# Performance work log

Hardware: AMD Instinct MI355X
Metric: run time of the kernel (lower is better)

The kernel has to match this reference:

```python
import jax, jax.numpy as jnp
import numpy as np

N_NODES = 100000
N_EDGES = 1600000
NUM_GRAPHS = 1000
NODE_IN, EDGE_IN = 32, 16
NODE_EMB, EDGE_EMB, HID, OUT, L = 64, 32, 64, 1, 3
EPS = 1e-5


def _glorot(key, shape):
    fan_in = shape[0]
    return jax.random.normal(key, shape, jnp.float32) / np.sqrt(fan_in)


def setup_inputs() -> dict:
    key = jax.random.key(0)
    ks = jax.random.split(key, 16)
    inp = {
        "x": jax.random.normal(ks[0], (N_NODES, NODE_IN), jnp.float32),
        "edge_attr": jax.random.normal(ks[1], (N_EDGES, EDGE_IN), jnp.float32),
        "edge_index": jax.random.randint(ks[2], (2, N_EDGES), 0, N_NODES, jnp.int64
                                         if jax.config.jax_enable_x64 else jnp.int32),
        "batch": jnp.sort(jax.random.randint(ks[3], (N_NODES,), 0, NUM_GRAPHS)),
        # embeddings
        "node_W": _glorot(ks[4], (NODE_IN, NODE_EMB)),
        "node_b": jnp.zeros((NODE_EMB,), jnp.float32),
        "edge_W": _glorot(ks[5], (EDGE_IN, EDGE_EMB)),
        "edge_b": jnp.zeros((EDGE_EMB,), jnp.float32),
        # per-layer MPNN params (node_dim==64 for every layer since node_emb_dim==hidden_dim)
        "msg_W": _glorot(ks[6], (L, NODE_EMB + EDGE_EMB, HID)),
        "msg_b": jnp.zeros((L, HID), jnp.float32),
        "msg_gamma": jnp.ones((L, HID), jnp.float32),
        "msg_beta": jnp.zeros((L, HID), jnp.float32),
        "upd_W": _glorot(ks[7], (L, NODE_EMB + HID, HID)),
        "upd_b": jnp.zeros((L, HID), jnp.float32),
        "upd_gamma": jnp.ones((L, HID), jnp.float32),
        "upd_beta": jnp.zeros((L, HID), jnp.float32),
        # readout
        "r1_W": _glorot(ks[8], (HID, HID)),
        "r1_b": jnp.zeros((HID,), jnp.float32),
        "r2_W": _glorot(ks[9], (HID, OUT)),
        "r2_b": jnp.zeros((OUT,), jnp.float32),
    }
    return inp


def _bn(h, gamma, beta):
    # BatchNorm1d in training mode: normalize with batch mean / biased variance
    mu = jnp.mean(h, axis=0)
    var = jnp.mean(jnp.square(h - mu), axis=0)
    return gamma * (h - mu) * jax.lax.rsqrt(var + EPS) + beta


def reference(x, edge_attr, edge_index, batch,
              node_W, node_b, edge_W, edge_b,
              msg_W, msg_b, msg_gamma, msg_beta,
              upd_W, upd_b, upd_gamma, upd_beta,
              r1_W, r1_b, r2_W, r2_b):
    h = x @ node_W + node_b                       # [N, 64]
    e = edge_attr @ edge_W + edge_b               # [E, 32]
    src, dst = edge_index[0], edge_index[1]
    for i in range(L):
        # message: gather x_j, concat edge feats, Linear-ReLU-BN (dropout = eval/no-op)
        m = jnp.concatenate([h[src], e], axis=-1) @ msg_W[i] + msg_b[i]   # [E, 64]
        m = _bn(jax.nn.relu(m), msg_gamma[i], msg_beta[i])
        # aggregate: scatter-add to destination nodes
        agg = jax.ops.segment_sum(m, dst, num_segments=N_NODES)          # [N, 64]
        # update: concat self feats, Linear-ReLU-BN
        u = jnp.concatenate([h, agg], axis=-1) @ upd_W[i] + upd_b[i]     # [N, 64]
        h = _bn(jax.nn.relu(u), upd_gamma[i], upd_beta[i])
    # global add pool over graphs
    g = jax.ops.segment_sum(h, batch, num_segments=NUM_GRAPHS)           # [G, 64]
    out = jax.nn.relu(g @ r1_W + r1_b) @ r2_W + r2_b                     # [G, 1]
    return out
```

## Files before the change

kernel.cpp:

```cpp
#include <hip/hip_runtime.h>
#include <hip/hip_bf16.h>

#define N_NODES   100000
#define N_EDGES   1600000
#define NUM_GRAPHS 1000

typedef unsigned int u32;
typedef unsigned short u16;

typedef __bf16 bf16_t;
typedef bf16_t bf16x8 __attribute__((ext_vector_type(8)));
typedef float  f32x4  __attribute__((ext_vector_type(4)));
typedef u32    u32x4  __attribute__((ext_vector_type(4)));

__device__ __forceinline__ float bf2f(u16 u){ return __uint_as_float(((u32)u)<<16); }
__device__ __forceinline__ float BL(u32 u){ return __uint_as_float(u<<16); }
__device__ __forceinline__ float BH(u32 u){ return __uint_as_float(u&0xffff0000u); }
__device__ __forceinline__ u16 f2bf(float f){
  u32 u = __float_as_uint(f);
  return (u16)((u + 0x7fffu + ((u>>16)&1u)) >> 16);
}
__device__ __forceinline__ float ldf(const void* p, size_t i, int isbf){
  return isbf ? bf2f(((const u16*)p)[i]) : ((const float*)p)[i];
}
__device__ __forceinline__ uint4 ntload4(const void* p){
  u32x4 v = __builtin_nontemporal_load((const u32x4*)p);
  return make_uint4(v.x, v.y, v.z, v.w);
}

union U4BF { uint4 u; bf16x8 v; };

__global__ void k_detect(const u32* __restrict__ x, int* __restrict__ flag){
  int t = threadIdx.x; int cnt = 0;
  for (int i = t; i < 256; i += 64){
    u32 w = x[i];
    u32 e = (w >> 7) & 0xffu;
    if (e >= 110u && e <= 137u) cnt++;
  }
  for (int o = 32; o; o >>= 1) cnt += __shfl_xor(cnt, o);
  if (t == 0) *flag = (cnt > 128) ? 1 : 0;
}

__global__ void k_idaff(float* __restrict__ haff){
  int c = threadIdx.x;
  haff[c] = 1.f; haff[64 + c] = 0.f;
}

__global__ void k_prep(const void* __restrict__ eW, const void* __restrict__ eb,
                       const void* __restrict__ mW, const void* __restrict__ mb,
                       u16* __restrict__ Weff, float* __restrict__ biasm,
                       const int* __restrict__ flagp){
  int isbf = *flagp;
  int l = blockIdx.x, c = threadIdx.x;
  u16* W = Weff + ((size_t)l*64 + c)*96;
  for (int k = 0; k < 64; k++)
    W[k] = f2bf(ldf(mW, (size_t)(l*96 + k)*64 + c, isbf));
  for (int j = 0; j < 16; j++){
    float acc = 0.f;
    for (int k = 0; k < 32; k++)
      acc += ldf(eW, (size_t)j*32 + k, isbf) * ldf(mW, (size_t)(l*96 + 64 + k)*64 + c, isbf);
    W[64 + j] = f2bf(acc);
  }
  float fbv = ldf(mb, (size_t)l*64 + c, isbf);
  for (int k = 0; k < 32; k++)
    fbv += ldf(eb, k, isbf) * ldf(mW, (size_t)(l*96 + 64 + k)*64 + c, isbf);
  W[80] = f2bf(fbv);
  biasm[(size_t)l*64 + c] = fbv;
  for (int k = 81; k < 96; k++) W[k] = 0;
}

__global__ void k_fold(const void* __restrict__ mW, const u16* __restrict__ Wbase,
                       const float* __restrict__ biasm, const float* __restrict__ haff,
                       u16* __restrict__ Wf, const int* __restrict__ flagp, int l){
  int isbf = *flagp; int c = threadIdx.x;
  const u16* Wb = Wbase + ((size_t)l*64 + c)*96;
  u16* W = Wf + (size_t)c*96;
  float bb = biasm[(size_t)l*64 + c];
  for (int k = 0; k < 64; k++){
    float w = ldf(mW, (size_t)(l*96 + k)*64 + c, isbf);
    W[k] = f2bf(haff[k] * w);
    bb = fmaf(haff[64 + k], w, bb);
  }
  for (int k = 64; k < 80; k++) W[k] = Wb[k];
  W[80] = f2bf(bb);
  for (int k = 81; k < 96; k++) W[k] = 0;
}

__global__ void k_updprep(const void* __restrict__ uW, const void* __restrict__ ub,
                          const float* __restrict__ maff, const float* __restrict__ haff,
                          u16* __restrict__ Wupd, float* __restrict__ biasv,
                          float* __restrict__ tvv, const int* __restrict__ flagp, int l){
  int isbf = *flagp; int c = threadIdx.x;
  u16* W = Wupd + (size_t)c*192;
  float tv = 0.f, bb = 0.f;
  for (int k = 0; k < 64; k++){
    float wka = ldf(uW, (size_t)(l*128 + k)*64 + c, isbf);
    W[k] = f2bf(haff[k] * wka);
    bb = fmaf(haff[64 + k], wka, bb);
    float wkb = ldf(uW, (size_t)(l*128 + 64 + k)*64 + c, isbf);
    float prod = wkb * maff[k];
    u16 hi = f2bf(prod);
    W[64 + k]  = hi;
    W[128 + k] = f2bf(prod - bf2f(hi));
    tv = fmaf(maff[64 + k], wkb, tv);
  }
  biasv[c] = ldf(ub, (size_t)l*64 + c, isbf) + bb;
  tvv[c] = tv;
}

__global__ void k_node_emb(const void* __restrict__ x, const void* __restrict__ nW,
                           const void* __restrict__ nb, u16* __restrict__ hsp,
                           const int* __restrict__ flagp){
  int isbf = *flagp;
  int lane = threadIdx.x & 63;
  int gw = (blockIdx.x*blockDim.x + threadIdx.x) >> 6;
  int nw = (gridDim.x*blockDim.x) >> 6;
  float w[32];
#pragma unroll
  for (int k = 0; k < 32; k++) w[k] = ldf(nW, (size_t)k*64 + lane, isbf);
  float bias = ldf(nb, lane, isbf);
  for (int n = gw; n < N_NODES; n += nw){
    float acc = bias;
    if (isbf){
      const uint4* xr = (const uint4*)((const u16*)x + (size_t)n*32);
#pragma unroll
      for (int q = 0; q < 4; q++){
        uint4 a = xr[q];
        u32 uu[4] = {a.x, a.y, a.z, a.w};
#pragma unroll
        for (int j = 0; j < 4; j++){
          acc = fmaf(BL(uu[j]), w[q*8 + 2*j + 0], acc);
          acc = fmaf(BH(uu[j]), w[q*8 + 2*j + 1], acc);
        }
      }
    } else {
      const float4* xr = (const float4*)((const float*)x + (size_t)n*32);
#pragma unroll
      for (int q = 0; q < 8; q++){
        float4 a = xr[q];
        acc = fmaf(a.x, w[q*4+0], acc); acc = fmaf(a.y, w[q*4+1], acc);
        acc = fmaf(a.z, w[q*4+2], acc); acc = fmaf(a.w, w[q*4+3], acc);
      }
    }
    u16 hi = f2bf(acc);
    hsp[(size_t)n*128 + lane]      = hi;
    hsp[(size_t)n*128 + 64 + lane] = f2bf(acc - bf2f(hi));
  }
}

__global__ void k_deg(const int* __restrict__ ei, int* __restrict__ deg){
  int i = blockIdx.x*blockDim.x + threadIdx.x;
  int stride = gridDim.x*blockDim.x;
  for (int e = i; e < N_EDGES; e += stride)
    atomicAdd(&deg[ei[N_EDGES + e]], 1);
}

__global__ void __launch_bounds__(256) k_scan1(const int* __restrict__ deg,
                                               int* __restrict__ bsum){
  __shared__ int wsum[4];
  int b = blockIdx.x, t = threadIdx.x;
  int i0 = b*512 + t;
  int s = 0;
  if (i0 < N_NODES) s += deg[i0];
  if (i0 + 256 < N_NODES) s += deg[i0 + 256];
  for (int o = 32; o; o >>= 1) s += __shfl_xor(s, o);
  if ((t & 63) == 0) wsum[t >> 6] = s;
  __syncthreads();
  if (t == 0) bsum[b] = wsum[0] + wsum[1] + wsum[2] + wsum[3];
}

__global__ void k_scan2(const int* __restrict__ bsum, int* __restrict__ boff,
                        int* __restrict__ rp){
  __shared__ int l[200];
  int t = threadIdx.x;
  if (t < 196) l[t] = bsum[t];
  __syncthreads();
  if (t == 0){
    int r = 0;
    for (int k = 0; k < 196; k++){ int x = l[k]; l[k] = r; r += x; }
    rp[N_NODES] = r;
  }
  __syncthreads();
  if (t < 196) boff[t] = l[t];
}

__global__ void __launch_bounds__(256) k_scan3(const int* __restrict__ deg,
                        const int* __restrict__ boff, int* __restrict__ rp,
                        int* __restrict__ cursor, float* __restrict__ degf){
  __shared__ int wpre[4];
  int b = blockIdx.x, t = threadIdx.x;
  int i0 = b*512 + 2*t;
  int d0 = (i0     < N_NODES) ? deg[i0]     : 0;
  int d1 = (i0 + 1 < N_NODES) ? deg[i0 + 1] : 0;
  int s = d0 + d1;
  int incl = s;
  for (int o = 1; o < 64; o <<= 1){ int u = __shfl_up(incl, o); if ((t & 63) >= o) incl += u; }
  if ((t & 63) == 63) wpre[t >> 6] = incl;
  __syncthreads();
  if (t == 0){ int r = 0; for (int k = 0; k < 4; k++){ int x = wpre[k]; wpre[k] = r; r += x; } }
  __syncthreads();
  int excl = boff[b] + wpre[t >> 6] + incl - s;
  if (i0 < N_NODES){
    rp[i0] = excl; cursor[i0] = excl; degf[i0] = (float)d0;
  }
  if (i0 + 1 < N_NODES){
    rp[i0+1] = excl + d0; cursor[i0+1] = excl + d0; degf[i0+1] = (float)d1;
  }
}

__global__ void k_ranges(const int* __restrict__ rp, int* __restrict__ wr,
                         int nwaves){
  int w = blockIdx.x*blockDim.x + threadIdx.x;
  if (w > nwaves) return;
  if (w == nwaves){ wr[w] = N_NODES; return; }
  long long t0 = (long long)w * N_EDGES / nwaves;
  int lo = 0, hi = N_NODES;
  while (lo < hi){ int mid = (lo+hi)>>1; if ((long long)rp[mid] < t0) lo = mid+1; else hi = mid; }
  wr[w] = lo;
}

__global__ void k_scatter(const int* __restrict__ ei, int* __restrict__ cursor,
                          int* __restrict__ perm2){
  int i = blockIdx.x*blockDim.x + threadIdx.x;
  int stride = gridDim.x*blockDim.x;
  for (int e = i; e < N_EDGES; e += stride){
    int d = ei[N_EDGES + e];
    int p = atomicAdd(&cursor[d], 1);
    ((int2*)perm2)[p] = make_int2(ei[e], e);
  }
}

__global__ void k_scatter2(const int* __restrict__ ei, int* __restrict__ cursor,
                           int* __restrict__ perm, u16* __restrict__ eacsr,
                           const void* __restrict__ ea, const int* __restrict__ flagp){
  int isbf = *flagp;
  int i = blockIdx.x*blockDim.x + threadIdx.x;
  int stride = gridDim.x*blockDim.x;
  if (i < 16){
    perm[N_EDGES + i] = 0;
    uint4 z = make_uint4(0,0,0,0);
    uint4* out = (uint4*)(eacsr + (size_t)(N_EDGES + i)*16);
    out[0] = z; out[1] = z;
  }
  for (int e = i; e < N_EDGES; e += stride){
    int d = ei[N_EDGES + e];
    int p = atomicAdd(&cursor[d], 1);
    perm[p] = ei[e];
    uint4 r0, r1;
    if (isbf){
      const uint4* er = (const uint4*)((const u16*)ea + (size_t)e*16);
      r0 = er[0]; r1 = er[1];
    } else {
      const float4* ef = (const float4*)((const float*)ea + (size_t)e*16);
      float4 f0 = ef[0], f1 = ef[1], f2 = ef[2], f3 = ef[3];
      r0.x = (u32)f2bf(f0.x) | ((u32)f2bf(f0.y)<<16);
      r0.y = (u32)f2bf(f0.z) | ((u32)f2bf(f0.w)<<16);
      r0.z = (u32)f2bf(f1.x) | ((u32)f2bf(f1.y)<<16);
      r0.w = (u32)f2bf(f1.z) | ((u32)f2bf(f1.w)<<16);
      r1.x = (u32)f2bf(f2.x) | ((u32)f2bf(f2.y)<<16);
      r1.y = (u32)f2bf(f2.z) | ((u32)f2bf(f2.w)<<16);
      r1.z = (u32)f2bf(f3.x) | ((u32)f2bf(f3.y)<<16);
      r1.w = (u32)f2bf(f3.z) | ((u32)f2bf(f3.w)<<16);
    }
    uint4* out = (uint4*)(eacsr + (size_t)p*16);
    out[0] = r0; out[1] = r1;
  }
}

__device__ __forceinline__ void adv_tile(const int* __restrict__ rp,
                                         int ni, int bi, int ei,
                                         int& no, int& bo, int& eo){
  if (bi + 16 < ei){ no = ni; bo = bi + 16; eo = ei; return; }
  int t = ni + 1;
  int nb = ei;
  int ne = rp[(t < N_NODES) ? t + 1 : N_NODES];
  while (nb == ne && t + 1 < N_NODES){
    t++; nb = ne; ne = rp[t + 1];
  }
  no = t; bo = nb; eo = ne;
}

__global__ void __launch_bounds__(256) k_msgmm(
    const u16* __restrict__ hsp, const void* __restrict__ ea,
    const int* __restrict__ rp, const int* __restrict__ perm2,
    const u16* __restrict__ Wl, u16* __restrict__ aggs,
    float* __restrict__ stats, const int* __restrict__ flagp,
    int nwaves){
  __shared__ float bs[128];
  int tid = threadIdx.x;
  if (tid < 128) bs[tid] = 0.f;
  __syncthreads();
  int isbf = *flagp;
  int lane = tid & 63, wv = tid >> 6;
  int w = blockIdx.x*4 + wv;
  long long t0 = (long long)w     * N_EDGES / nwaves;
  long long t1 = (long long)(w+1) * N_EDGES / nwaves;
  int lo = 0, hi = N_NODES;
  while (lo < hi){ int mid = (lo+hi)>>1; if ((long long)rp[mid] < t0) lo = mid+1; else hi = mid; }
  int n0 = lo, n1;
  if (w == nwaves-1) n1 = N_NODES;
  else {
    lo = 0; hi = N_NODES;
    while (lo < hi){ int mid = (lo+hi)>>1; if ((long long)rp[mid] < t1) lo = mid+1; else hi = mid; }
    n1 = lo;
  }
  int nn = lane & 15, kg = lane >> 4;
  bf16x8 B[3][4];
#pragma unroll
  for (int t = 0; t < 4; t++)
#pragma unroll
    for (int kb = 0; kb < 3; kb++)
      B[kb][t] = *(const bf16x8*)(Wl + (size_t)(t*16+nn)*96 + kb*32 + kg*8);
  U4BF ac; ac.u = make_uint4((kg==2)? 0x3f80u : 0u, 0u, 0u, 0u);
  float s1[4] = {0,0,0,0}, s2[4] = {0,0,0,0};
  for (int n = n0; n < n1; n++){
    int b0 = rp[n], b1 = rp[n+1];
    float r0 = 0.f, r1 = 0.f, r2 = 0.f, r3 = 0.f;
    for (int base = b0; base < b1; base += 16){
      int rem = b1 - base; if (rem > 16) rem = 16;
      int row = (nn < rem) ? nn : rem-1;
      int2 p = ((const int2*)perm2)[base + row];
      const uint4* hp = (const uint4*)(hsp + (size_t)p.x*128);
      U4BF fA, fB, fC;
      fA.u = hp[kg];
      fB.u = hp[4 + kg];
      if (kg < 2){
        if (isbf){
          fC.u = ((const uint4*)ea)[(size_t)p.y*2 + kg];
        } else {
          const float4* ef = (const float4*)ea;
          float4 f0 = ef[(size_t)p.y*4 + kg*2];
          float4 f1 = ef[(size_t)p.y*4 + kg*2 + 1];
          fC.u.x = (u32)f2bf(f0.x) | ((u32)f2bf(f0.y)<<16);
          fC.u.y = (u32)f2bf(f0.z) | ((u32)f2bf(f0.w)<<16);
          fC.u.z = (u32)f2bf(f1.x) | ((u32)f2bf(f1.y)<<16);
          fC.u.w = (u32)f2bf(f1.z) | ((u32)f2bf(f1.w)<<16);
        }
      } else fC = ac;
      f32x4 a0 = {0,0,0,0}, a1 = {0,0,0,0}, a2 = {0,0,0,0}, a3 = {0,0,0,0};
      a0 = __builtin_amdgcn_mfma_f32_16x16x32_bf16(fA.v, B[0][0], a0, 0,0,0);
      a1 = __builtin_amdgcn_mfma_f32_16x16x32_bf16(fA.v, B[0][1], a1, 0,0,0);
      a2 = __builtin_amdgcn_mfma_f32_16x16x32_bf16(fA.v, B[0][2], a2, 0,0,0);
      a3 = __builtin_amdgcn_mfma_f32_16x16x32_bf16(fA.v, B[0][3], a3, 0,0,0);
      a0 = __builtin_amdgcn_mfma_f32_16x16x32_bf16(fB.v, B[1][0], a0, 0,0,0);
      a1 = __builtin_amdgcn_mfma_f32_16x16x32_bf16(fB.v, B[1][1], a1, 0,0,0);
      a2 = __builtin_amdgcn_mfma_f32_16x16x32_bf16(fB.v, B[1][2], a2, 0,0,0);
      a3 = __builtin_amdgcn_mfma_f32_16x16x32_bf16(fB.v, B[1][3], a3, 0,0,0);
      a0 = __builtin_amdgcn_mfma_f32_16x16x32_bf16(fC.v, B[2][0], a0, 0,0,0);
      a1 = __builtin_amdgcn_mfma_f32_16x16x32_bf16(fC.v, B[2][1], a1, 0,0,0);
      a2 = __builtin_amdgcn_mfma_f32_16x16x32_bf16(fC.v, B[2][2], a2, 0,0,0);
      a3 = __builtin_amdgcn_mfma_f32_16x16x32_bf16(fC.v, B[2][3], a3, 0,0,0);
      int rowbase = kg*4;
      float ts0 = 0.f, ts1 = 0.f, ts2 = 0.f, ts3 = 0.f;
#pragma unroll
      for (int j = 0; j < 4; j++){
        bool valid = (rowbase + j) < rem;
        float m0 = fmaxf(a0[j], 0.f); m0 = valid ? m0 : 0.f;
        float m1 = fmaxf(a1[j], 0.f); m1 = valid ? m1 : 0.f;
        float m2 = fmaxf(a2[j], 0.f); m2 = valid ? m2 : 0.f;
        float m3 = fmaxf(a3[j], 0.f); m3 = valid ? m3 : 0.f;
        ts0 += m0; ts1 += m1; ts2 += m2; ts3 += m3;
        s2[0] = fmaf(m0,m0,s2[0]); s2[1] = fmaf(m1,m1,s2[1]);
        s2[2] = fmaf(m2,m2,s2[2]); s2[3] = fmaf(m3,m3,s2[3]);
      }
      s1[0] += ts0; s1[1] += ts1; s1[2] += ts2; s1[3] += ts3;
      ts0 += __shfl_xor(ts0,16); ts0 += __shfl_xor(ts0,32);
      ts1 += __shfl_xor(ts1,16); ts1 += __shfl_xor(ts1,32);
      ts2 += __shfl_xor(ts2,16); ts2 += __shfl_xor(ts2,32);
      ts3 += __shfl_xor(ts3,16); ts3 += __shfl_xor(ts3,32);
      r0 += ts0; r1 += ts1; r2 += ts2; r3 += ts3;
    }
    float v = (kg==0) ? r0 : (kg==1) ? r1 : (kg==2) ? r2 : r3;
    u16 hiv = f2bf(v);
    aggs[(size_t)n*128 + lane]      = hiv;
    aggs[(size_t)n*128 + 64 + lane] = f2bf(v - bf2f(hiv));
  }
#pragma unroll
  for (int t = 0; t < 4; t++){
    atomicAdd(&bs[t*16+nn], s1[t]);
    atomicAdd(&bs[64+t*16+nn], s2[t]);
  }
  __syncthreads();
  if (tid < 128) atomicAdd(&stats[tid], bs[tid]);
}

__global__ void __launch_bounds__(256) k_msgmm2(
    const u16* __restrict__ hsp, const u16* __restrict__ eacsr,
    const int* __restrict__ rp, const int* __restrict__ perm,
    const u16* __restrict__ Wl, u16* __restrict__ aggs,
    float* __restrict__ stats, const int* __restrict__ wranges){
  __shared__ float bs[128];
  int tid = threadIdx.x;
  if (tid < 128) bs[tid] = 0.f;
  __syncthreads();
  int lane = tid & 63;
  int w = blockIdx.x*4 + (tid >> 6);
  int nBeg = wranges[w], nEnd = wranges[w+1];
  int nn = lane & 15, kg = lane >> 4;
  bf16x8 B[3][4];
#pragma unroll
  for (int t = 0; t < 4; t++)
#pragma unroll
    for (int kb = 0; kb < 3; kb++)
      B[kb][t] = *(const bf16x8*)(Wl + (size_t)(t*16+nn)*96 + kb*32 + kg*8);
  U4BF ac; ac.u = make_uint4((kg==2)? 0x3f80u : 0u, 0u, 0u, 0u);
  float s1[4] = {0,0,0,0}, s2[4] = {0,0,0,0};

  if (nBeg < nEnd){
    {
      int pv = rp[nBeg];
      for (int m = nBeg; m < nEnd; m++){
        int nx = rp[m+1];
        if (nx == pv){
          aggs[(size_t)m*128 + lane] = 0;
          aggs[(size_t)m*128 + 64 + lane] = 0;
        }
        pv = nx;
      }
    }
    int nA = nBeg;
    int baseA = rp[nA], b1A = rp[nA+1];
    while (baseA == b1A && nA + 1 < nEnd){ nA++; baseA = b1A; b1A = rp[nA+1]; }
    if (baseA < b1A){
      int nB, baseB, b1B;
      adv_tile(rp, nA, baseA, b1A, nB, baseB, b1B);
      int pB = __builtin_nontemporal_load(&perm[baseB + nn]);
      U4BF fAA, fAB, fAC;
      {
        int pA = __builtin_nontemporal_load(&perm[baseA + nn]);
        const uint4* hpA = (const uint4*)(hsp + (size_t)pA*128);
        fAA.u = hpA[kg]; fAB.u = hpA[4 + kg];
        if (kg < 2) fAC.u = ntload4(eacsr + ((size_t)baseA + nn)*16 + (size_t)kg*8);
        else fAC = ac;
      }
      float r0 = 0.f, r1 = 0.f, r2 = 0.f, r3 = 0.f;
      while (true){
        int nC, baseC, b1C;
        adv_tile(rp, nB, baseB, b1B, nC, baseC, b1C);
        int pC = __builtin_nontemporal_load(&perm[baseC + nn]);
        const uint4* hpB = (const uint4*)(hsp + (size_t)pB*128);
        U4BF fBA, fBB, fBC;
        fBA.u = hpB[kg]; fBB.u = hpB[4 + kg];
        if (kg < 2) fBC.u = ntload4(eacsr + ((size_t)baseB + nn)*16 + (size_t)kg*8);
        else fBC = ac;
        f32x4 a0 = {0,0,0,0}, a1 = {0,0,0,0}, a2 = {0,0,0,0}, a3 = {0,0,0,0};
        a0 = __builtin_amdgcn_mfma_f32_16x16x32_bf16(fAA.v, B[0][0], a0, 0,0,0);
        a1 = __builtin_amdgcn_mfma_f32_16x16x32_bf16(fAA.v, B[0][1], a1, 0,0,0);
        a2 = __builtin_amdgcn_mfma_f32_16x16x32_bf16(fAA.v, B[0][2], a2, 0,0,0);
        a3 = __builtin_amdgcn_mfma_f32_16x16x32_bf16(fAA.v, B[0][3], a3, 0,0,0);
        a0 = __builtin_amdgcn_mfma_f32_16x16x32_bf16(fAB.v, B[1][0], a0, 0,0,0);
        a1 = __builtin_amdgcn_mfma_f32_16x16x32_bf16(fAB.v, B[1][1], a1, 0,0,0);
        a2 = __builtin_amdgcn_mfma_f32_16x16x32_bf16(fAB.v, B[1][2], a2, 0,0,0);
        a3 = __builtin_amdgcn_mfma_f32_16x16x32_bf16(fAB.v, B[1][3], a3, 0,0,0);
        a0 = __builtin_amdgcn_mfma_f32_16x16x32_bf16(fAC.v, B[2][0], a0, 0,0,0);
        a1 = __builtin_amdgcn_mfma_f32_16x16x32_bf16(fAC.v, B[2][1], a1, 0,0,0);
        a2 = __builtin_amdgcn_mfma_f32_16x16x32_bf16(fAC.v, B[2][2], a2, 0,0,0);
        a3 = __builtin_amdgcn_mfma_f32_16x16x32_bf16(fAC.v, B[2][3], a3, 0,0,0);
        int rem = b1A - baseA; if (rem > 16) rem = 16;
        int rowbase = kg*4;
        float ts0 = 0.f, ts1 = 0.f, ts2 = 0.f, ts3 = 0.f;
#pragma unroll
        for (int j = 0; j < 4; j++){
          bool valid = (rowbase + j) < rem;
          float m0 = fmaxf(a0[j], 0.f); m0 = valid ? m0 : 0.f;
          float m1 = fmaxf(a1[j], 0.f); m1 = valid ? m1 : 0.f;
          float m2 = fmaxf(a2[j], 0.f); m2 = valid ? m2 : 0.f;
          float m3 = fmaxf(a3[j], 0.f); m3 = valid ? m3 : 0.f;
          ts0 += m0; ts1 += m1; ts2 += m2; ts3 += m3;
          s2[0] = fmaf(m0,m0,s2[0]); s2[1] = fmaf(m1,m1,s2[1]);
          s2[2] = fmaf(m2,m2,s2[2]); s2[3] = fmaf(m3,m3,s2[3]);
        }
        s1[0] += ts0; s1[1] += ts1; s1[2] += ts2; s1[3] += ts3;
        r0 += ts0; r1 += ts1; r2 += ts2; r3 += ts3;
        if (baseA + 16 >= b1A){
          r0 += __shfl_xor(r0,16); r0 += __shfl_xor(r0,32);
          r1 += __shfl_xor(r1,16); r1 += __shfl_xor(r1,32);
          r2 += __shfl_xor(r2,16); r2 += __shfl_xor(r2,32);
          r3 += __shfl_xor(r3,16); r3 += __shfl_xor(r3,32);
          float v = (kg==0) ? r0 : (kg==1) ? r1 : (kg==2) ? r2 : r3;
          u16 hiv = f2bf(v);
          aggs[(size_t)nA*128 + lane]      = hiv;
          aggs[(size_t)nA*128 + 64 + lane] = f2bf(v - bf2f(hiv));
          r0 = r1 = r2 = r3 = 0.f;
        }
        nA = nB; baseA = baseB; b1A = b1B;
        fAA = fBA; fAB = fBB; fAC = fBC;
        nB = nC; baseB = baseC; b1B = b1C; pB = pC;
        if (nA >= nEnd) break;
      }
    }
  }
#pragma unroll
  for (int t = 0; t < 4; t++){
    atomicAdd(&bs[t*16+nn], s1[t]);
    atomicAdd(&bs[64+t*16+nn], s2[t]);
  }
  __syncthreads();
  if (tid < 128) atomicAdd(&stats[tid], bs[tid]);
}

__global__ void k_fin(float* __restrict__ stats, const void* __restrict__ gamma,
                      const void* __restrict__ beta, float* __restrict__ aff,
                      float cnt_inv, int goff, const int* __restrict__ flagp){
  int isbf = *flagp; int c = threadIdx.x;
  float mu  = stats[c]      * cnt_inv;
  float var = stats[64 + c] * cnt_inv - mu*mu;
  float rs  = rsqrtf(var + 1e-5f);
  float g = ldf(gamma, (size_t)goff + c, isbf);
  float b = ldf(beta,  (size_t)goff + c, isbf);
  aff[c]      = g*rs;
  aff[64 + c] = b - g*mu*rs;
  stats[c] = 0.f; stats[64 + c] = 0.f;
}

#define UPD_TILES (N_NODES/16)
__global__ void __launch_bounds__(256) k_updmm(
    const u16* __restrict__ hsp, u16* __restrict__ aggs,
    const float* __restrict__ degf, const u16* __restrict__ Wupd,
    const float* __restrict__ biasv, const float* __restrict__ tvv,
    float* __restrict__ stats){
  __shared__ float bs[128];
  int tid = threadIdx.x;
  if (tid < 128) bs[tid] = 0.f;
  __syncthreads();
  int lane = tid & 63;
  int nn = lane & 15, kg = lane >> 4;
  int w = blockIdx.x*4 + (tid >> 6);
  int nwv = gridDim.x*4;
  bf16x8 B[6][4];
#pragma unroll
  for (int t = 0; t < 4; t++)
#pragma unroll
    for (int kb = 0; kb < 6; kb++)
      B[kb][t] = *(const bf16x8*)(Wupd + (size_t)(t*16+nn)*192 + kb*32 + kg*8);
  float bc[4], tc[4];
#pragma unroll
  for (int t = 0; t < 4; t++){ bc[t] = biasv[t*16+nn]; tc[t] = tvv[t*16+nn]; }
  float s1[4] = {0,0,0,0}, s2[4] = {0,0,0,0};
  for (int tile = w; tile < UPD_TILES; tile += nwv){
    int n0 = tile*16;
    int r = n0 + nn;
    const uint4* hp = (const uint4*)hsp;
    const uint4* ap = (const uint4*)aggs;
    U4BF hh0, hh1, hl0, hl1, ah0, ah1, al0, al1;
    hh0.u = ntload4(&hp[(size_t)r*16 + kg]);       hh1.u = ntload4(&hp[(size_t)r*16 + 4 + kg]);
    hl0.u = ntload4(&hp[(size_t)r*16 + 8 + kg]);   hl1.u = ntload4(&hp[(size_t)r*16 + 12 + kg]);
    ah0.u = ntload4(&ap[(size_t)r*16 + kg]);       ah1.u = ntload4(&ap[(size_t)r*16 + 4 + kg]);
    al0.u = ntload4(&ap[(size_t)r*16 + 8 + kg]);   al1.u = ntload4(&ap[(size_t)r*16 + 12 + kg]);
    float dg[4];
#pragma unroll
    for (int j = 0; j < 4; j++) dg[j] = degf[n0 + kg*4 + j];
    f32x4 a0 = {0,0,0,0}, a1 = {0,0,0,0}, a2 = {0,0,0,0}, a3 = {0,0,0,0};
#define MF(F,KB) \
    a0 = __builtin_amdgcn_mfma_f32_16x16x32_bf16(F.v, B[KB][0], a0, 0,0,0); \
    a1 = __builtin_amdgcn_mfma_f32_16x16x32_bf16(F.v, B[KB][1], a1, 0,0,0); \
    a2 = __builtin_amdgcn_mfma_f32_16x16x32_bf16(F.v, B[KB][2], a2, 0,0,0); \
    a3 = __builtin_amdgcn_mfma_f32_16x16x32_bf16(F.v, B[KB][3], a3, 0,0,0);
    MF(hh0,0) MF(hh1,1) MF(hl0,0) MF(hl1,1)
    MF(ah0,2) MF(ah1,3) MF(ah0,4) MF(ah1,5)
    MF(al0,2) MF(al1,3)
#undef MF
#pragma unroll
    for (int j = 0; j < 4; j++){
      int n = n0 + kg*4 + j;
      float m0 = fmaxf(fmaf(tc[0], dg[j], a0[j] + bc[0]), 0.f);
      float m1 = fmaxf(fmaf(tc[1], dg[j], a1[j] + bc[1]), 0.f);
      float m2 = fmaxf(fmaf(tc[2], dg[j], a2[j] + bc[2]), 0.f);
      float m3 = fmaxf(fmaf(tc[3], dg[j], a3[j] + bc[3]), 0.f);
      s1[0] += m0; s1[1] += m1; s1[2] += m2; s1[3] += m3;
      s2[0] = fmaf(m0,m0,s2[0]); s2[1] = fmaf(m1,m1,s2[1]);
      s2[2] = fmaf(m2,m2,s2[2]); s2[3] = fmaf(m3,m3,s2[3]);
      u16* hw = aggs + (size_t)n*128;
      u16 q0 = f2bf(m0), q1 = f2bf(m1), q2 = f2bf(m2), q3 = f2bf(m3);
      hw[     nn] = q0;  hw[64 +      nn] = f2bf(m0 - bf2f(q0));
      hw[16 + nn] = q1;  hw[64 + 16 + nn] = f2bf(m1 - bf2f(q1));
      hw[32 + nn] = q2;  hw[64 + 32 + nn] = f2bf(m2 - bf2f(q2));
      hw[48 + nn] = q3;  hw[64 + 48 + nn] = f2bf(m3 - bf2f(q3));
    }
  }
#pragma unroll
  for (int t = 0; t < 4; t++){
    atomicAdd(&bs[t*16+nn], s1[t]);
    atomicAdd(&bs[64+t*16+nn], s2[t]);
  }
  __syncthreads();
  if (tid < 128) atomicAdd(&stats[tid], bs[tid]);
}

__global__ void k_pool(const u16* __restrict__ hsp, const int* __restrict__ batch,
                       const float* __restrict__ aff, float* __restrict__ g){
  int lane = threadIdx.x & 63;
  int gw = (blockIdx.x*blockDim.x + threadIdx.x) >> 6;
  int nw = (gridDim.x*blockDim.x) >> 6;
  float s = aff[lane], t = aff[64 + lane];
  int chunk = (N_NODES + nw - 1) / nw;
  int n0 = gw*chunk;
  int n1 = n0 + chunk; if (n1 > N_NODES) n1 = N_NODES;
  int cur = -1; float acc = 0.f, cnt = 0.f;
  for (int n = n0; n < n1; n++){
    int b = batch[n];
    float v = bf2f(hsp[(size_t)n*128 + lane]) + bf2f(hsp[(size_t)n*128 + 64 + lane]);
    if (b != cur){
      if (cur >= 0) atomicAdd(&g[(size_t)cur*64 + lane], fmaf(s, acc, t*cnt));
      cur = b; acc = v; cnt = 1.f;
    } else { acc += v; cnt += 1.f; }
  }
  if (cur >= 0) atomicAdd(&g[(size_t)cur*64 + lane], fmaf(s, acc, t*cnt));
}

__global__ void k_read(const float* __restrict__ g, const void* __restrict__ r1W,
                       const void* __restrict__ r1b, const void* __restrict__ r2W,
                       const void* __restrict__ r2b, void* __restrict__ out,
                       const int* __restrict__ flagp){
  int isbf = *flagp;
  int lane = threadIdx.x;
  int gr = blockIdx.x;
  float w[64];
#pragma unroll
  for (int k = 0; k < 64; k++) w[k] = ldf(r1W, (size_t)k*64 + lane, isbf);
  float acc = ldf(r1b, lane, isbf);
  const float4* grow = (const float4*)(g + (size_t)gr*64);
#pragma unroll
  for (int q = 0; q < 16; q++){
    float4 a = grow[q];
    acc = fmaf(a.x, w[4*q+0], acc); acc = fmaf(a.y, w[4*q+1], acc);
    acc = fmaf(a.z, w[4*q+2], acc); acc = fmaf(a.w, w[4*q+3], acc);
  }
  float hid = fmaxf(acc, 0.f);
  float p = hid * ldf(r2W, lane, isbf);
  for (int o = 32; o; o >>= 1) p += __shfl_xor(p, o);
  if (lane == 0){
    float v = p + ldf(r2b, 0, isbf);
    if (isbf) ((__hip_bfloat16*)out)[gr] = __float2bfloat16(v);
    else      ((float*)out)[gr] = v;
  }
}

extern "C" void kernel_launch(void* const* d_in, const int* in_sizes, int n_in,
                              void* d_out, int out_size, void* d_ws, size_t ws_size,
                              hipStream_t stream){
  const void* x    = d_in[0];
  const void* ea   = d_in[1];
  const int*  ei   = (const int*)d_in[2];
  const int*  bt   = (const int*)d_in[3];
  const void* nW   = d_in[4];  const void* nb  = d_in[5];
  const void* eW   = d_in[6];  const void* eb  = d_in[7];
  const void* mW   = d_in[8];  const void* mb  = d_in[9];
  const void* mg   = d_in[10]; const void* mbe = d_in[11];
  const void* uW   = d_in[12]; const void* ub  = d_in[13];
  const void* ug   = d_in[14]; const void* ube = d_in[15];
  const void* r1W  = d_in[16]; const void* r1b = d_in[17];
  const void* r2W  = d_in[18]; const void* r2b = d_in[19];

  const size_t NEED_BIG = 110768044ull;
  const bool big = (ws_size >= NEED_BIG);

  float* ws = (float*)d_ws;
  size_t off = 0;
  auto alloc = [&](size_t n){ float* p = ws + off; off += n; return p; };

  u16*   hsp   = (u16*)alloc(6400000);
  u16*   aggs  = (u16*)alloc(6400000);
  u16*   eacsr = nullptr; int* perm = nullptr; int* perm2 = nullptr;
  if (big){
    eacsr = (u16*)alloc(12800128);
    perm  = (int*)alloc(1600016);
  } else {
    perm2 = (int*)alloc(3200000);
  }
  float* degf   = alloc(100000);
  float* zero0  = ws + off;
  int*   deg_i  = (int*)alloc(100000);
  float* g      = alloc(64000);
  float* mstats = alloc(128);
  float* ustats = alloc(128);
  size_t zeroN  = (size_t)((ws + off) - zero0);
  float* maff   = alloc(128);
  float* haff   = alloc(128);
  int*   flag   = (int*)alloc(16);
  u16*   Weff   = (u16*)alloc(9216);
  u16*   Wfold  = (u16*)alloc(3072);
  u16*   Wupd   = (u16*)alloc(6144);
  float* biasm  = alloc(192);
  float* biasv  = alloc(64);
  float* tvv    = alloc(64);
  int*   row_ptr= (int*)alloc(100001);
  int*   cursor = (int*)alloc(100000);
  int*   bsum   = (int*)alloc(196);
  int*   boff   = (int*)alloc(196);
  int*   wrng   = (int*)alloc(8194);

  const int MM_BLOCKS = 2048;
  const int MM_WAVES  = MM_BLOCKS * 4;
  const int UPD_BLOCKS = 782;

  k_detect<<<1, 64, 0, stream>>>((const u32*)x, flag);
  hipMemsetAsync(zero0, 0, zeroN*sizeof(float), stream);
  k_idaff<<<1, 64, 0, stream>>>(haff);
  k_prep<<<3, 64, 0, stream>>>(eW, eb, mW, mb, Weff, biasm, flag);
  k_node_emb<<<256, 256, 0, stream>>>(x, nW, nb, hsp, flag);
  k_deg<<<512, 256, 0, stream>>>(ei, deg_i);
  k_scan1<<<196, 256, 0, stream>>>(deg_i, bsum);
  k_scan2<<<1, 256, 0, stream>>>(bsum, boff, row_ptr);
  k_scan3<<<196, 256, 0, stream>>>(deg_i, boff, row_ptr, cursor, degf);
  if (big){
    k_ranges<<<33, 256, 0, stream>>>(row_ptr, wrng, MM_WAVES);
    k_scatter2<<<512, 256, 0, stream>>>(ei, cursor, perm, eacsr, ea, flag);
  } else {
    k_scatter<<<512, 256, 0, stream>>>(ei, cursor, perm2);
  }

  u16* H = hsp;
  u16* G = aggs;
  for (int l = 0; l < 3; l++){
    k_fold<<<1, 64, 0, stream>>>(mW, Weff, biasm, haff, Wfold, flag, l);
    if (big)
      k_msgmm2<<<MM_BLOCKS, 256, 0, stream>>>(H, eacsr, row_ptr, perm, Wfold,
                                              G, mstats, wrng);
    else
      k_msgmm<<<MM_BLOCKS, 256, 0, stream>>>(H, ea, row_ptr, perm2, Wfold,
                                             G, mstats, flag, MM_WAVES);
    k_fin<<<1, 64, 0, stream>>>(mstats, mg, mbe, maff, 1.0f/(float)N_EDGES, l*64, flag);
    k_updprep<<<1, 64, 0, stream>>>(uW, ub, maff, haff, Wupd, biasv, tvv, flag, l);
    k_updmm<<<UPD_BLOCKS, 256, 0, stream>>>(H, G, degf, Wupd, biasv, tvv, ustats);
    k_fin<<<1, 64, 0, stream>>>(ustats, ug, ube, haff, 1.0f/(float)N_NODES, l*64, flag);
    u16* tmp = H; H = G; G = tmp;
  }

  k_pool<<<128, 256, 0, stream>>>(H, bt, haff, g);
  k_read<<<NUM_GRAPHS, 64, 0, stream>>>(g, r1W, r1b, r2W, r2b, d_out, flag);
}
```

Baseline: 1.368 ms.

## Precompute per-wave 16-edge tile lists for the message GEMM loop

Adds three setup kernels that count, prefix-scan and fill a packed list of 16-edge tiles per wave, each entry holding node id, row count and a last-tile flag. The message kernel then walks this flat list instead of advancing through row_ptr with the adv_tile logic, which removes dependent row_ptr loads and branching from the inner pipelined loop. It also swaps the nontemporal loads for plain loads and pads the perm and edge-attribute buffers further so prefetches two tiles ahead stay in bounds. The cost is three extra small launches, a larger workspace requirement and a serial scan in one block.

```diff
diff --git a/kernel.cpp b/kernel.cpp
--- a/kernel.cpp
+++ b/kernel.cpp
@@ -219,6 +219,59 @@
   wr[w] = lo;
 }
 
+
+__global__ void k_tcnt(const int* __restrict__ rp, const int* __restrict__ wr,
+                       int* __restrict__ tcnt, int nwaves){
+  int w = blockIdx.x*blockDim.x + threadIdx.x;
+  if (w >= nwaves) return;
+  int n0 = wr[w], n1 = wr[w+1];
+  int c = 0;
+  for (int n = n0; n < n1; n++){
+    int d = rp[n+1] - rp[n];
+    c += (d + 15) >> 4;
+  }
+  tcnt[w] = c;
+}
+
+__global__ void k_tscan(const int* __restrict__ tcnt, int* __restrict__ twoff,
+                        int nwaves){
+  __shared__ int ps[256];
+  int t = threadIdx.x;
+  int s = 0;
+  for (int i = 0; i < 32; i++) s += tcnt[t*32 + i];
+  ps[t] = s;
+  __syncthreads();
+  if (t == 0){
+    int r = 0;
+    for (int k = 0; k < 256; k++){ int x = ps[k]; ps[k] = r; r += x; }
+    twoff[nwaves] = r;
+  }
+  __syncthreads();
+  int off = ps[t];
+  for (int i = 0; i < 32; i++){
+    twoff[t*32 + i] = off;
+    off += tcnt[t*32 + i];
+  }
+}
+
+__global__ void k_tfill(const int* __restrict__ rp, const int* __restrict__ wr,
+                        const int* __restrict__ twoff, int* __restrict__ tlist,
+                        int nwaves){
+  int w = blockIdx.x*blockDim.x + threadIdx.x;
+  if (w >= nwaves) return;
+  int n0 = wr[w], n1 = wr[w+1];
+  int o = twoff[w];
+  for (int n = n0; n < n1; n++){
+    int b = rp[n], e = rp[n+1];
+    while (b < e){
+      int rem = e - b; if (rem > 16) rem = 16;
+      int last = (b + 16 >= e) ? 1 : 0;
+      tlist[o++] = (n << 5) | ((rem - 1) << 1) | last;
+      b += 16;
+    }
+  }
+}
+
 __global__ void k_scatter(const int* __restrict__ ei, int* __restrict__ cursor,
                           int* __restrict__ perm2){
   int i = blockIdx.x*blockDim.x + threadIdx.x;
@@ -236,7 +289,7 @@
   int isbf = *flagp;
   int i = blockIdx.x*blockDim.x + threadIdx.x;
   int stride = gridDim.x*blockDim.x;
-  if (i < 16){
+  if (i < 48){
     perm[N_EDGES + i] = 0;
     uint4 z = make_uint4(0,0,0,0);
     uint4* out = (uint4*)(eacsr + (size_t)(N_EDGES + i)*16);
@@ -384,18 +437,18 @@
   if (tid < 128) atomicAdd(&stats[tid], bs[tid]);
 }
 
-__global__ void __launch_bounds__(256) k_msgmm2(
+__global__ void __launch_bounds__(256) k_msgmm3(
     const u16* __restrict__ hsp, const u16* __restrict__ eacsr,
     const int* __restrict__ rp, const int* __restrict__ perm,
     const u16* __restrict__ Wl, u16* __restrict__ aggs,
-    float* __restrict__ stats, const int* __restrict__ wranges){
+    float* __restrict__ stats, const int* __restrict__ wranges,
+    const int* __restrict__ twoff, const int* __restrict__ tlist){
   __shared__ float bs[128];
   int tid = threadIdx.x;
   if (tid < 128) bs[tid] = 0.f;
   __syncthreads();
   int lane = tid & 63;
   int w = blockIdx.x*4 + (tid >> 6);
-  int nBeg = wranges[w], nEnd = wranges[w+1];
   int nn = lane & 15, kg = lane >> 4;
   bf16x8 B[3][4];
 #pragma unroll
@@ -406,88 +459,88 @@
   U4BF ac; ac.u = make_uint4((kg==2)? 0x3f80u : 0u, 0u, 0u, 0u);
   float s1[4] = {0,0,0,0}, s2[4] = {0,0,0,0};
 
+  int nBeg = wranges[w], nEnd = wranges[w+1];
   if (nBeg < nEnd){
+    int pv = rp[nBeg];
+    for (int m = nBeg; m < nEnd; m++){
+      int nx = rp[m+1];
+      if (nx == pv){
+        aggs[(size_t)m*128 + lane] = 0;
+        aggs[(size_t)m*128 + 64 + lane] = 0;
+      }
+      pv = nx;
+    }
+  }
+
+  int tB = twoff[w], tE = twoff[w+1];
+  if (tB < tE){
+    int recA = tlist[tB];
+    int baseA = rp[nBeg];
+    int recB = (tB+1 < tE) ? tlist[tB+1] : recA;
+    int baseB = baseA + ((recA>>1)&15) + 1;
+    U4BF fAA, fAB, fAC;
     {
-      int pv = rp[nBeg];
-      for (int m = nBeg; m < nEnd; m++){
-        int nx = rp[m+1];
-        if (nx == pv){
-          aggs[(size_t)m*128 + lane] = 0;
-          aggs[(size_t)m*128 + 64 + lane] = 0;
-        }
-        pv = nx;
+      int pA = perm[baseA + nn];
+      const uint4* hpA = (const uint4*)(hsp + (size_t)pA*128);
+      fAA.u = hpA[kg]; fAB.u = hpA[4 + kg];
+      if (kg < 2) fAC.u = *(const uint4*)(eacsr + ((size_t)baseA + nn)*16 + (size_t)kg*8);
+      else fAC = ac;
+    }
+    int pB = perm[baseB + nn];
+    float r0 = 0.f, r1 = 0.f, r2 = 0.f, r3 = 0.f;
+    for (int i = tB; i < tE; i++){
+      int recC = (i+2 < tE) ? tlist[i+2] : recB;
+      int baseC = baseB + ((recB>>1)&15) + 1;
+      int pC = perm[baseC + nn];
+      const uint4* hpB = (const uint4*)(hsp + (size_t)pB*128);
+      U4BF fBA, fBB, fBC;
+      fBA.u = hpB[kg]; fBB.u = hpB[4 + kg];
+      if (kg < 2) fBC.u = *(const uint4*)(eacsr + ((size_t)baseB + nn)*16 + (size_t)kg*8);
+      else fBC = ac;
+      f32x4 a0 = {0,0,0,0}, a1 = {0,0,0,0}, a2 = {0,0,0,0}, a3 = {0,0,0,0};
+      a0 = __builtin_amdgcn_mfma_f32_16x16x32_bf16(fAA.v, B[0][0], a0, 0,0,0);
+      a1 = __builtin_amdgcn_mfma_f32_16x16x32_bf16(fAA.v, B[0][1], a1, 0,0,0);
+      a2 = __builtin_amdgcn_mfma_f32_16x16x32_bf16(fAA.v, B[0][2], a2, 0,0,0);
+      a3 = __builtin_amdgcn_mfma_f32_16x16x32_bf16(fAA.v, B[0][3], a3, 0,0,0);
+      a0 = __builtin_amdgcn_mfma_f32_16x16x32_bf16(fAB.v, B[1][0], a0, 0,0,0);
+      a1 = __builtin_amdgcn_mfma_f32_16x16x32_bf16(fAB.v, B[1][1], a1, 0,0,0);
+      a2 = __builtin_amdgcn_mfma_f32_16x16x32_bf16(fAB.v, B[1][2], a2, 0,0,0);
+      a3 = __builtin_amdgcn_mfma_f32_16x16x32_bf16(fAB.v, B[1][3], a3, 0,0,0);
+      a0 = __builtin_amdgcn_mfma_f32_16x16x32_bf16(fAC.v, B[2][0], a0, 0,0,0);
+      a1 = __builtin_amdgcn_mfma_f32_16x16x32_bf16(fAC.v, B[2][1], a1, 0,0,0);
+      a2 = __builtin_amdgcn_mfma_f32_16x16x32_bf16(fAC.v, B[2][2], a2, 0,0,0);
+      a3 = __builtin_amdgcn_mfma_f32_16x16x32_bf16(fAC.v, B[2][3], a3, 0,0,0);
+      int rem = ((recA >> 1) & 15) + 1;
+      int rowbase = kg*4;
+      float ts0 = 0.f, ts1 = 0.f, ts2 = 0.f, ts3 = 0.f;
+#pragma unroll
+      for (int j = 0; j < 4; j++){
+        bool valid = (rowbase + j) < rem;
+        float m0 = fmaxf(a0[j], 0.f); m0 = valid ? m0 : 0.f;
+        float m1 = fmaxf(a1[j], 0.f); m1 = valid ? m1 : 0.f;
+        float m2 = fmaxf(a2[j], 0.f); m2 = valid ? m2 : 0.f;
+        float m3 = fmaxf(a3[j], 0.f); m3 = valid ? m3 : 0.f;
+        ts0 += m0; ts1 += m1; ts2 += m2; ts3 += m3;
+        s2[0] = fmaf(m0,m0,s2[0]); s2[1] = fmaf(m1,m1,s2[1]);
+        s2[2] = fmaf(m2,m2,s2[2]); s2[3] = fmaf(m3,m3,s2[3]);
       }
-    }
-    int nA = nBeg;
-    int baseA = rp[nA], b1A = rp[nA+1];
-    while (baseA == b1A && nA + 1 < nEnd){ nA++; baseA = b1A; b1A = rp[nA+1]; }
-    if (baseA < b1A){
-      int nB, baseB, b1B;
-      adv_tile(rp, nA, baseA, b1A, nB, baseB, b1B);
-      int pB = __builtin_nontemporal_load(&perm[baseB + nn]);
-      U4BF fAA, fAB, fAC;
-      {
-        int pA = __builtin_nontemporal_load(&perm[baseA + nn]);
-        const uint4* hpA = (const uint4*)(hsp + (size_t)pA*128);
-        fAA.u = hpA[kg]; fAB.u = hpA[4 + kg];
-        if (kg < 2) fAC.u = ntload4(eacsr + ((size_t)baseA + nn)*16 + (size_t)kg*8);
-        else fAC = ac;
+      s1[0] += ts0; s1[1] += ts1; s1[2] += ts2; s1[3] += ts3;
+      r0 += ts0; r1 += ts1; r2 += ts2; r3 += ts3;
+      if (recA & 1){
+        r0 += __shfl_xor(r0,16); r0 += __shfl_xor(r0,32);
+        r1 += __shfl_xor(r1,16); r1 += __shfl_xor(r1,32);
+        r2 += __shfl_xor(r2,16); r2 += __shfl_xor(r2,32);
+        r3 += __shfl_xor(r3,16); r3 += __shfl_xor(r3,32);
+        float v = (kg==0) ? r0 : (kg==1) ? r1 : (kg==2) ? r2 : r3;
+        int node = recA >> 5;
+        u16 hiv = f2bf(v);
+        aggs[(size_t)node*128 + lane]      = hiv;
+        aggs[(size_t)node*128 + 64 + lane] = f2bf(v - bf2f(hiv));
+        r0 = r1 = r2 = r3 = 0.f;
       }
-      float r0 = 0.f, r1 = 0.f, r2 = 0.f, r3 = 0.f;
-      while (true){
-        int nC, baseC, b1C;
-        adv_tile(rp, nB, baseB, b1B, nC, baseC, b1C);
-        int pC = __builtin_nontemporal_load(&perm[baseC + nn]);
-        const uint4* hpB = (const uint4*)(hsp + (size_t)pB*128);
-        U4BF fBA, fBB, fBC;
-        fBA.u = hpB[kg]; fBB.u = hpB[4 + kg];
-        if (kg < 2) fBC.u = ntload4(eacsr + ((size_t)baseB + nn)*16 + (size_t)kg*8);
-        else fBC = ac;
-        f32x4 a0 = {0,0,0,0}, a1 = {0,0,0,0}, a2 = {0,0,0,0}, a3 = {0,0,0,0};
-        a0 = __builtin_amdgcn_mfma_f32_16x16x32_bf16(fAA.v, B[0][0], a0, 0,0,0);
-        a1 = __builtin_amdgcn_mfma_f32_16x16x32_bf16(fAA.v, B[0][1], a1, 0,0,0);
-        a2 = __builtin_amdgcn_mfma_f32_16x16x32_bf16(fAA.v, B[0][2], a2, 0,0,0);
-        a3 = __builtin_amdgcn_mfma_f32_16x16x32_bf16(fAA.v, B[0][3], a3, 0,0,0);
-        a0 = __builtin_amdgcn_mfma_f32_16x16x32_bf16(fAB.v, B[1][0], a0, 0,0,0);
-        a1 = __builtin_amdgcn_mfma_f32_16x16x32_bf16(fAB.v, B[1][1], a1, 0,0,0);
-        a2 = __builtin_amdgcn_mfma_f32_16x16x32_bf16(fAB.v, B[1][2], a2, 0,0,0);
-        a3 = __builtin_amdgcn_mfma_f32_16x16x32_bf16(fAB.v, B[1][3], a3, 0,0,0);
-        a0 = __builtin_amdgcn_mfma_f32_16x16x32_bf16(fAC.v, B[2][0], a0, 0,0,0);
-        a1 = __builtin_amdgcn_mfma_f32_16x16x32_bf16(fAC.v, B[2][1], a1, 0,0,0);
-        a2 = __builtin_amdgcn_mfma_f32_16x16x32_bf16(fAC.v, B[2][2], a2, 0,0,0);
-        a3 = __builtin_amdgcn_mfma_f32_16x16x32_bf16(fAC.v, B[2][3], a3, 0,0,0);
-        int rem = b1A - baseA; if (rem > 16) rem = 16;
-        int rowbase = kg*4;
-        float ts0 = 0.f, ts1 = 0.f, ts2 = 0.f, ts3 = 0.f;
-#pragma unroll
-        for (int j = 0; j < 4; j++){
-          bool valid = (rowbase + j) < rem;
-          float m0 = fmaxf(a0[j], 0.f); m0 = valid ? m0 : 0.f;
-          float m1 = fmaxf(a1[j], 0.f); m1 = valid ? m1 : 0.f;
-          float m2 = fmaxf(a2[j], 0.f); m2 = valid ? m2 : 0.f;
-          float m3 = fmaxf(a3[j], 0.f); m3 = valid ? m3 : 0.f;
-          ts0 += m0; ts1 += m1; ts2 += m2; ts3 += m3;
-          s2[0] = fmaf(m0,m0,s2[0]); s2[1] = fmaf(m1,m1,s2[1]);
-          s2[2] = fmaf(m2,m2,s2[2]); s2[3] = fmaf(m3,m3,s2[3]);
-        }
-        s1[0] += ts0; s1[1] += ts1; s1[2] += ts2; s1[3] += ts3;
-        r0 += ts0; r1 += ts1; r2 += ts2; r3 += ts3;
-        if (baseA + 16 >= b1A){
-          r0 += __shfl_xor(r0,16); r0 += __shfl_xor(r0,32);
-          r1 += __shfl_xor(r1,16); r1 += __shfl_xor(r1,32);
-          r2 += __shfl_xor(r2,16); r2 += __shfl_xor(r2,32);
-          r3 += __shfl_xor(r3,16); r3 += __shfl_xor(r3,32);
-          float v = (kg==0) ? r0 : (kg==1) ? r1 : (kg==2) ? r2 : r3;
-          u16 hiv = f2bf(v);
-          aggs[(size_t)nA*128 + lane]      = hiv;
-          aggs[(size_t)nA*128 + 64 + lane] = f2bf(v - bf2f(hiv));
-          r0 = r1 = r2 = r3 = 0.f;
-        }
-        nA = nB; baseA = baseB; b1A = b1B;
-        fAA = fBA; fAB = fBB; fAC = fBC;
-        nB = nC; baseB = baseC; b1B = b1C; pB = pC;
-        if (nA >= nEnd) break;
-      }
+      recA = recB; baseA = baseB;
+      fAA = fBA; fAB = fBB; fAC = fBC;
+      recB = recC; baseB = baseC; pB = pC;
     }
   }
 #pragma unroll
@@ -652,7 +705,7 @@
   const void* r1W  = d_in[16]; const void* r1b = d_in[17];
   const void* r2W  = d_in[18]; const void* r2b = d_in[19];
 
-  const size_t NEED_BIG = 110768044ull;
+  const size_t NEED_BIG = 111634736ull;
   const bool big = (ws_size >= NEED_BIG);
 
   float* ws = (float*)d_ws;
@@ -662,9 +715,10 @@
   u16*   hsp   = (u16*)alloc(6400000);
   u16*   aggs  = (u16*)alloc(6400000);
   u16*   eacsr = nullptr; int* perm = nullptr; int* perm2 = nullptr;
+  int*   tcnt = nullptr; int* twoff = nullptr; int* tlist = nullptr;
   if (big){
-    eacsr = (u16*)alloc(12800128);
-    perm  = (int*)alloc(1600016);
+    eacsr = (u16*)alloc(12800384);
+    perm  = (int*)alloc(1600048);
   } else {
     perm2 = (int*)alloc(3200000);
   }
@@ -689,6 +743,11 @@
   int*   bsum   = (int*)alloc(196);
   int*   boff   = (int*)alloc(196);
   int*   wrng   = (int*)alloc(8194);
+  if (big){
+    tcnt  = (int*)alloc(8192);
+    twoff = (int*)alloc(8193);
+    tlist = (int*)alloc(200000);
+  }
 
   const int MM_BLOCKS = 2048;
   const int MM_WAVES  = MM_BLOCKS * 4;
@@ -705,6 +764,9 @@
   k_scan3<<<196, 256, 0, stream>>>(deg_i, boff, row_ptr, cursor, degf);
   if (big){
     k_ranges<<<33, 256, 0, stream>>>(row_ptr, wrng, MM_WAVES);
+    k_tcnt<<<32, 256, 0, stream>>>(row_ptr, wrng, tcnt, MM_WAVES);
+    k_tscan<<<1, 256, 0, stream>>>(tcnt, twoff, MM_WAVES);
+    k_tfill<<<32, 256, 0, stream>>>(row_ptr, wrng, twoff, tlist, MM_WAVES);
     k_scatter2<<<512, 256, 0, stream>>>(ei, cursor, perm, eacsr, ea, flag);
   } else {
     k_scatter<<<512, 256, 0, stream>>>(ei, cursor, perm2);
@@ -715,8 +777,8 @@
   for (int l = 0; l < 3; l++){
     k_fold<<<1, 64, 0, stream>>>(mW, Weff, biasm, haff, Wfold, flag, l);
     if (big)
-      k_msgmm2<<<MM_BLOCKS, 256, 0, stream>>>(H, eacsr, row_ptr, perm, Wfold,
-                                              G, mstats, wrng);
+      k_msgmm3<<<MM_BLOCKS, 256, 0, stream>>>(H, eacsr, row_ptr, perm, Wfold,
+                                              G, mstats, wrng, twoff, tlist);
     else
       k_msgmm<<<MM_BLOCKS, 256, 0, stream>>>(H, ea, row_ptr, perm2, Wfold,
                                              G, mstats, flag, MM_WAVES);
```

New measurement: 1.319 ms. -3.6%, faster.
